# Kernel tuning notes

Hardware: AMD Instinct MI355X
Metric: run time of the kernel (lower is better)

Reference implementation:

```python
import jax, jax.numpy as jnp
import numpy as np

T, H, I, E, K = 4096, 1024, 2048, 32, 4


def setup_inputs() -> dict:
    key = jax.random.key(0)
    ks = jax.random.split(key, 8)
    s = lambda k, shape, std: (jax.random.normal(k, shape, jnp.float32) * std)
    return {
        "x": s(ks[0], (T, H), 1.0),
        "router_w": s(ks[1], (E, H), 0.02),
        "gate_w": s(ks[2], (E, H, I), 0.02),
        "up_w": s(ks[3], (E, H, I), 0.02),
        "down_w": s(ks[4], (E, I, H), 0.02),
        "shared_gate_w": s(ks[5], (H, I), 0.02),
        "shared_up_w": s(ks[6], (H, I), 0.02),
        "shared_down_w": s(ks[7], (I, H), 0.02),
        "top_k": K,
    }


def _moe_forward(x, router_w, gate_w, up_w, down_w, sg, su, sd, top_k):
    # x: [T, H]; expert weights: gate/up [E, H, I], down [E, I, H]
    Tn = x.shape[0]
    En = router_w.shape[0]

    # Router: softmax over experts, top-k selection, renormalize selected probs
    logits = x @ router_w.T                                   # [T, E]
    probs = jax.nn.softmax(logits, axis=-1)
    topk_p, topk_i = jax.lax.top_k(probs, top_k)              # [T, K]
    topk_p = topk_p / jnp.sum(topk_p, axis=-1, keepdims=True)

    # Dense combine weights: combine[t, e] = routing weight of expert e for token t
    combine = jnp.zeros((Tn, En), x.dtype).at[
        jnp.arange(Tn)[:, None], topk_i].add(topk_p)          # [T, E]

    def expert_step(acc, inp):
        wg, wu, wd, c = inp                                   # [H,I], [H,I], [I,H], [T]
        h = jax.nn.silu(x @ wg) * (x @ wu)                    # [T, I] SwiGLU
        return acc + c[:, None] * (h @ wd), None

    acc0 = jnp.zeros_like(x)
    out, _ = jax.lax.scan(expert_step, acc0,
                          (gate_w, up_w, down_w, combine.T))

    # Shared expert: always applied
    shared = (jax.nn.silu(x @ sg) * (x @ su)) @ sd            # [T, H]
    return out + shared


def reference(x, router_w, gate_w, up_w, down_w,
              shared_gate_w, shared_up_w, shared_down_w, top_k):
    return _moe_forward(x, router_w, gate_w, up_w, down_w,
                        shared_gate_w, shared_up_w, shared_down_w, top_k)
```

## Files before the change

### kernel.cpp

```cpp
#include <hip/hip_runtime.h>
#include <hip/hip_bf16.h>

#define T_TOK 4096
#define H_DIM 1024
#define I_DIM 2048
#define N_EXP 32
#define TOPK  4
#define TKTOT (T_TOK * TOPK)
#define ROWS_MAX 24576
#define MAX_TILES 192
#define BM 128
#define BK 64
#define WMAT ((size_t)I_DIM * H_DIM)

typedef _Float16 f16;
typedef __attribute__((ext_vector_type(4))) f16  f16x4;
typedef __attribute__((ext_vector_type(8))) f16  f16x8;
typedef __attribute__((ext_vector_type(4))) float f32x4;

__device__ __forceinline__ void glds16(const f16* g, f16* l) {
  __builtin_amdgcn_global_load_lds(
      (const __attribute__((address_space(1))) void*)g,
      (__attribute__((address_space(3))) void*)l, 16, 0, 0);
}
__device__ __forceinline__ void sfence() { __builtin_amdgcn_sched_barrier(0); }
__device__ __forceinline__ void bar_vm0() {
  sfence();
  asm volatile("s_waitcnt vmcnt(0) lgkmcnt(0)" ::: "memory");
  sfence();
  __builtin_amdgcn_s_barrier();
  sfence();
}

__global__ void prep_kernel(const float* __restrict__ x, f16* __restrict__ xb,
                            int* __restrict__ row_token,
                            int* __restrict__ counts) {
  int gid = blockIdx.x * blockDim.x + threadIdx.x;
  float4 v = *(const float4*)(x + (size_t)gid * 4);
  f16x4 hv = { (f16)v.x, (f16)v.y, (f16)v.z, (f16)v.w };
  *(f16x4*)(xb + (size_t)gid * 4) = hv;
  if (gid < ROWS_MAX) row_token[gid] = (gid < T_TOK) ? gid : 0;
  if (gid < N_EXP) counts[gid] = 0;
}

__global__ __launch_bounds__(256) void tcvt_kernel(
    const float* __restrict__ src, const float* __restrict__ ssrc,
    f16* __restrict__ dst, int R, int C, int tilesC) {
  int per = (R >> 6) * tilesC;
  int mat = blockIdx.x / per, rem = blockIdx.x % per;
  int r0 = (rem / tilesC) << 6, c0 = (rem % tilesC) << 6;
  const float* s = (mat < N_EXP ? src + (size_t)mat * R * C : ssrc)
                   + (size_t)r0 * C + c0;
  f16* d = dst + (size_t)mat * R * C + (size_t)c0 * R + r0;

  __shared__ float t[64][65];
  int tid = threadIdx.x;
  int rr = tid >> 2, cc = (tid & 3) * 16;
#pragma unroll
  for (int j = 0; j < 4; ++j) {
    float4 v = *(const float4*)(s + (size_t)rr * C + cc + 4 * j);
    t[rr][cc + 4 * j + 0] = v.x; t[rr][cc + 4 * j + 1] = v.y;
    t[rr][cc + 4 * j + 2] = v.z; t[rr][cc + 4 * j + 3] = v.w;
  }
  __syncthreads();
  f16x8 o0, o1;
#pragma unroll
  for (int j = 0; j < 8; ++j) o0[j] = (f16)t[cc + j][rr];
#pragma unroll
  for (int j = 0; j < 8; ++j) o1[j] = (f16)t[cc + 8 + j][rr];
  *(f16x8*)(d + (size_t)rr * R + cc) = o0;
  *(f16x8*)(d + (size_t)rr * R + cc + 8) = o1;
}

__global__ void router_kernel(const float* __restrict__ x,
                              const float* __restrict__ rw,
                              int* __restrict__ expert_sel,
                              float* __restrict__ weight_sel,
                              int* __restrict__ counts) {
  int wid = threadIdx.x >> 6, lane = threadIdx.x & 63;
  int t = blockIdx.x * 4 + wid;
  float xr[16];
#pragma unroll
  for (int j = 0; j < 16; ++j) xr[j] = x[(size_t)t * H_DIM + lane + j * 64];
  float l[32];
#pragma unroll
  for (int e = 0; e < 32; ++e) {
    float p = 0.f;
#pragma unroll
    for (int j = 0; j < 16; ++j) p += xr[j] * rw[(size_t)e * H_DIM + lane + j * 64];
#pragma unroll
    for (int off = 32; off; off >>= 1) p += __shfl_xor(p, off, 64);
    l[e] = p;
  }
  if (lane == 0) {
    unsigned used = 0;
    int sel[4]; float lv[4];
#pragma unroll
    for (int k = 0; k < 4; ++k) {
      float bv = -3.4e38f; int bi = 0;
#pragma unroll
      for (int e = 0; e < 32; ++e) {
        bool better = (((used >> e) & 1u) == 0u) && (l[e] > bv);
        bv = better ? l[e] : bv;
        bi = better ? e : bi;
      }
      used |= 1u << bi; sel[k] = bi; lv[k] = bv;
    }
    float m = lv[0];
    float p0 = __expf(lv[0] - m), p1 = __expf(lv[1] - m);
    float p2 = __expf(lv[2] - m), p3 = __expf(lv[3] - m);
    float s = p0 + p1 + p2 + p3;
    float wv[4] = { p0 / s, p1 / s, p2 / s, p3 / s };
#pragma unroll
    for (int k = 0; k < 4; ++k) {
      expert_sel[t * 4 + k] = sel[k];
      weight_sel[t * 4 + k] = wv[k];
      atomicAdd(&counts[sel[k]], 1);
    }
  }
}

__global__ void scan_kernel(const int* __restrict__ counts, int* __restrict__ cursor,
                            int* __restrict__ tile_expert, int* __restrict__ tile_row0,
                            int* __restrict__ ntiles) {
  int lane = threadIdx.x;
  if (lane < T_TOK / BM) { tile_expert[lane] = N_EXP; tile_row0[lane] = lane * BM; }
  int nte = 0, rows = 0;
  if (lane < N_EXP) {
    int c = counts[lane];
    nte = (c + BM - 1) / BM;
    rows = nte * BM;
  }
  int pnte = nte, prows = rows;
#pragma unroll
  for (int off = 1; off < 64; off <<= 1) {
    int t1 = __shfl_up(pnte, off, 64);
    int t2 = __shfl_up(prows, off, 64);
    if (lane >= off) { pnte += t1; prows += t2; }
  }
  int excl_nte = pnte - nte, excl_rows = prows - rows;
  if (lane < N_EXP) {
    int pos = T_TOK + excl_rows;
    cursor[lane] = pos;
    int tb = T_TOK / BM + excl_nte;
    for (int i = 0; i < nte; ++i) {
      tile_expert[tb + i] = lane;
      tile_row0[tb + i] = pos + i * BM;
    }
    if (lane == N_EXP - 1) ntiles[0] = tb + nte;
  }
}

__global__ void scatter_kernel(const int* __restrict__ expert_sel,
                               int* __restrict__ cursor,
                               int* __restrict__ row_token,
                               int* __restrict__ slot_of) {
  int i = blockIdx.x * blockDim.x + threadIdx.x;
  if (i >= TKTOT) return;
  int e = expert_sel[i];
  int pos = atomicAdd(&cursor[e], 1);
  row_token[pos] = i >> 2;
  slot_of[i] = pos;
}

__global__ __launch_bounds__(256, 2) void gemm1_kernel(
    const f16* __restrict__ xb,
    const f16* __restrict__ gT, const f16* __restrict__ uT,
    const int* __restrict__ row_token,
    const int* __restrict__ tile_expert, const int* __restrict__ tile_row0,
    const int* __restrict__ ntiles, f16* __restrict__ hbuf) {
  int d = blockIdx.y * gridDim.x + blockIdx.x;
  int l = (d & 7) * 768 + (d >> 3);
  int bx = l % MAX_TILES;
  int n0 = (l / MAX_TILES) * 64;
  if (bx >= ntiles[0]) return;
  int e = tile_expert[bx];
  int row0 = tile_row0[bx];
  const f16* wg = gT + (size_t)e * WMAT;
  const f16* wu = uT + (size_t)e * WMAT;

  __shared__ __align__(16) f16 smem[2 * 16384];
  f16 (*Ct)[72] = (f16(*)[72])smem;

  int tid = threadIdx.x;
  int lane = tid & 63, wid = tid >> 6;
  int wm = wid >> 1, wn = wid & 1;
  int lr = lane & 15, lk = (lane >> 4) * 8;

  const f16* abase[4];
#pragma unroll
  for (int it = 0; it < 4; ++it) {
    int idx = tid + it * 256;
    int arow = idx >> 3, sl = idx & 7;
    abase[it] = xb + (size_t)row_token[row0 + arow] * H_DIM + ((sl ^ (arow & 7)) << 3);
  }
  const f16* gbase[2];
  const f16* ubase[2];
#pragma unroll
  for (int it = 0; it < 2; ++it) {
    int idx = tid + it * 256;
    int brow = idx >> 3, sl = idx & 7;
    size_t off = (size_t)(n0 + brow) * H_DIM + ((sl ^ (brow & 7)) << 3);
    gbase[it] = wg + off;
    ubase[it] = wu + off;
  }

  f32x4 accg[4][2], accu[4][2];
#pragma unroll
  for (int m = 0; m < 4; ++m)
#pragma unroll
    for (int n = 0; n < 2; ++n) { accg[m][n] = (f32x4)0.f; accu[m][n] = (f32x4)0.f; }

  const int NK = H_DIM / BK;

#define G1_ISSUE(K0, BUF)                                                    \
  {                                                                          \
    f16* Ab = smem + (BUF) * 16384;                                          \
    f16* Bgb = Ab + 8192;                                                    \
    f16* Bub = Bgb + 4096;                                                   \
    sfence();                                                                \
    _Pragma("unroll")                                                        \
    for (int it = 0; it < 4; ++it)                                           \
      glds16(abase[it] + (K0), Ab + (tid + it * 256) * 8);                   \
    _Pragma("unroll")                                                        \
    for (int it = 0; it < 2; ++it) {                                         \
      glds16(gbase[it] + (K0), Bgb + (tid + it * 256) * 8);                  \
      glds16(ubase[it] + (K0), Bub + (tid + it * 256) * 8);                  \
    }                                                                        \
    sfence();                                                                \
  }

  G1_ISSUE(0, 0);
  for (int ks = 0; ks < NK; ++ks) {
    int buf = ks & 1;
    bar_vm0();
    if (ks + 1 < NK) G1_ISSUE((ks + 1) * BK, buf ^ 1);
    const f16* Ab = smem + buf * 16384;
    const f16* Bgb = Ab + 8192;
    const f16* Bub = Bgb + 4096;
    __builtin_amdgcn_s_setprio(1);
#pragma unroll
    for (int kk = 0; kk < BK; kk += 32) {
      f16x8 a[4], bg[2], bu[2];
#pragma unroll
      for (int m = 0; m < 4; ++m) {
        int ar = wm * 64 + m * 16 + lr;
        a[m] = *(const f16x8*)(Ab + ar * BK + ((kk + lk) ^ ((ar & 7) << 3)));
      }
#pragma unroll
      for (int n = 0; n < 2; ++n) {
        int rowb = wn * 32 + n * 16 + lr;
        int ko = (kk + lk) ^ ((rowb & 7) << 3);
        bg[n] = *(const f16x8*)(Bgb + rowb * BK + ko);
        bu[n] = *(const f16x8*)(Bub + rowb * BK + ko);
      }
#pragma unroll
      for (int m = 0; m < 4; ++m)
#pragma unroll
        for (int n = 0; n < 2; ++n) {
          accg[m][n] = __builtin_amdgcn_mfma_f32_16x16x32_f16(a[m], bg[n], accg[m][n], 0, 0, 0);
          accu[m][n] = __builtin_amdgcn_mfma_f32_16x16x32_f16(a[m], bu[n], accu[m][n], 0, 0, 0);
        }
    }
    __builtin_amdgcn_s_setprio(0);
  }
#undef G1_ISSUE

  __syncthreads();
#pragma unroll
  for (int m = 0; m < 4; ++m)
#pragma unroll
    for (int n = 0; n < 2; ++n)
#pragma unroll
      for (int j = 0; j < 4; ++j) {
        float g = accg[m][n][j], u = accu[m][n][j];
        float hv = g / (1.f + __expf(-g)) * u;
        Ct[wm * 64 + m * 16 + (lane >> 4) * 4 + j][wn * 32 + n * 16 + lr] = (f16)hv;
      }
  __syncthreads();
#pragma unroll
  for (int it = 0; it < 4; ++it) {
    int idx = tid + it * 256;
    int r = idx >> 3, g8 = (idx & 7) * 8;
    *(f16x8*)(hbuf + (size_t)(row0 + r) * I_DIM + n0 + g8) = *(const f16x8*)&Ct[r][g8];
  }
}

__global__ __launch_bounds__(256, 2) void gemm2_kernel(
    const f16* __restrict__ hbuf,
    const f16* __restrict__ dT,
    const int* __restrict__ tile_expert, const int* __restrict__ tile_row0,
    const int* __restrict__ ntiles, f16* __restrict__ ybuf) {
  int d = blockIdx.y * gridDim.x + blockIdx.x;
  int l = (d & 7) * 192 + (d >> 3);
  int bx = l % MAX_TILES;
  int n0 = (l / MAX_TILES) * 128;
  if (bx >= ntiles[0]) return;
  int e = tile_expert[bx];
  int row0 = tile_row0[bx];
  const f16* wd = dT + (size_t)e * WMAT;

  __shared__ __align__(16) f16 smem[2 * 16384];
  f16 (*Ct)[136] = (f16(*)[136])smem;

  int tid = threadIdx.x;
  int lane = tid & 63, wid = tid >> 6;
  int wm = wid >> 1, wn = wid & 1;
  int lr = lane & 15, lk = (lane >> 4) * 8;

  const f16* abase[4];
  const f16* bbase[4];
#pragma unroll
  for (int it = 0; it < 4; ++it) {
    int idx = tid + it * 256;
    int arow = idx >> 3, sl = idx & 7;
    abase[it] = hbuf + (size_t)(row0 + arow) * I_DIM + ((sl ^ (arow & 7)) << 3);
    bbase[it] = wd + (size_t)(n0 + arow) * I_DIM + ((sl ^ (arow & 7)) << 3);
  }

  f32x4 acc[4][4];
#pragma unroll
  for (int m = 0; m < 4; ++m)
#pragma unroll
    for (int n = 0; n < 4; ++n) acc[m][n] = (f32x4)0.f;

  const int NK = I_DIM / BK;

#define G2_ISSUE(K0, BUF)                                                    \
  {                                                                          \
    f16* Ab = smem + (BUF) * 16384;                                          \
    f16* Bb = Ab + 8192;                                                     \
    sfence();                                                                \
    _Pragma("unroll")                                                        \
    for (int it = 0; it < 4; ++it) {                                         \
      glds16(abase[it] + (K0), Ab + (tid + it * 256) * 8);                   \
      glds16(bbase[it] + (K0), Bb + (tid + it * 256) * 8);                   \
    }                                                                        \
    sfence();                                                                \
  }

  G2_ISSUE(0, 0);
  for (int ks = 0; ks < NK; ++ks) {
    int buf = ks & 1;
    bar_vm0();
    if (ks + 1 < NK) G2_ISSUE((ks + 1) * BK, buf ^ 1);
    const f16* Ab = smem + buf * 16384;
    const f16* Bb = Ab + 8192;
    __builtin_amdgcn_s_setprio(1);
#pragma unroll
    for (int kk = 0; kk < BK; kk += 32) {
      f16x8 a[4], bd[4];
#pragma unroll
      for (int m = 0; m < 4; ++m) {
        int ar = wm * 64 + m * 16 + lr;
        a[m] = *(const f16x8*)(Ab + ar * BK + ((kk + lk) ^ ((ar & 7) << 3)));
      }
#pragma unroll
      for (int n = 0; n < 4; ++n) {
        int rowb = wn * 64 + n * 16 + lr;
        bd[n] = *(const f16x8*)(Bb + rowb * BK + ((kk + lk) ^ ((rowb & 7) << 3)));
      }
#pragma unroll
      for (int m = 0; m < 4; ++m)
#pragma unroll
        for (int n = 0; n < 4; ++n)
          acc[m][n] = __builtin_amdgcn_mfma_f32_16x16x32_f16(a[m], bd[n], acc[m][n], 0, 0, 0);
    }
    __builtin_amdgcn_s_setprio(0);
  }
#undef G2_ISSUE

  __syncthreads();
#pragma unroll
  for (int m = 0; m < 4; ++m)
#pragma unroll
    for (int n = 0; n < 4; ++n)
#pragma unroll
      for (int j = 0; j < 4; ++j)
        Ct[wm * 64 + m * 16 + (lane >> 4) * 4 + j][wn * 64 + n * 16 + lr] =
            (f16)acc[m][n][j];
  __syncthreads();
#pragma unroll
  for (int it = 0; it < 8; ++it) {
    int idx = tid + it * 256;
    int r = idx >> 4, g8 = (idx & 15) * 8;
    *(f16x8*)(ybuf + (size_t)(row0 + r) * H_DIM + n0 + g8) = *(const f16x8*)&Ct[r][g8];
  }
}

__global__ void gather_kernel(const f16* __restrict__ ybuf,
                              const int* __restrict__ slot_of,
                              const float* __restrict__ weight_sel,
                              float* __restrict__ out) {
  int gid = blockIdx.x * blockDim.x + threadIdx.x;
  int t = gid >> 7, s8 = (gid & 127) * 8;
  f16x8 ysh = *(const f16x8*)(ybuf + (size_t)t * H_DIM + s8);
  float a[8];
#pragma unroll
  for (int j = 0; j < 8; ++j) a[j] = (float)ysh[j];
#pragma unroll
  for (int k = 0; k < 4; ++k) {
    int sl = slot_of[t * 4 + k];
    float w = weight_sel[t * 4 + k];
    f16x8 v = *(const f16x8*)(ybuf + (size_t)sl * H_DIM + s8);
#pragma unroll
    for (int j = 0; j < 8; ++j) a[j] += w * (float)v[j];
  }
  float4 o0 = { a[0], a[1], a[2], a[3] };
  float4 o1 = { a[4], a[5], a[6], a[7] };
  *(float4*)(out + (size_t)t * H_DIM + s8) = o0;
  *(float4*)(out + (size_t)t * H_DIM + s8 + 4) = o1;
}

extern "C" void kernel_launch(void* const* d_in, const int* in_sizes, int n_in,
                              void* d_out, int out_size, void* d_ws, size_t ws_size,
                              hipStream_t stream) {
  const float* x        = (const float*)d_in[0];
  const float* router_w = (const float*)d_in[1];
  const float* gate_w   = (const float*)d_in[2];
  const float* up_w     = (const float*)d_in[3];
  const float* down_w   = (const float*)d_in[4];
  const float* sgw      = (const float*)d_in[5];
  const float* suw      = (const float*)d_in[6];
  const float* sdw      = (const float*)d_in[7];
  float* out = (float*)d_out;

  char* w = (char*)d_ws;
  f16*   xb         = (f16*)w;   w += (size_t)T_TOK * H_DIM * 2;
  int*   expert_sel = (int*)w;   w += (size_t)TKTOT * 4;
  float* weight_sel = (float*)w; w += (size_t)TKTOT * 4;
  int*   slot_of    = (int*)w;   w += (size_t)TKTOT * 4;
  int*   counts     = (int*)w;   w += 256;
  int*   cursor     = (int*)w;   w += 256;
  int*   tile_exp   = (int*)w;   w += MAX_TILES * 4;
  int*   tile_row0  = (int*)w;   w += MAX_TILES * 4;
  int*   ntiles     = (int*)w;   w += 256;
  int*   row_token  = (int*)w;   w += (size_t)ROWS_MAX * 4;
  f16*   hbuf       = (f16*)w;   w += (size_t)ROWS_MAX * I_DIM * 2;
  f16*   ybuf       = (f16*)w;   w += (size_t)ROWS_MAX * H_DIM * 2;
  f16*   gT         = (f16*)w;   w += (size_t)(N_EXP + 1) * WMAT * 2;
  f16*   uT         = (f16*)w;   w += (size_t)(N_EXP + 1) * WMAT * 2;
  f16*   dT         = (f16*)w;   w += (size_t)(N_EXP + 1) * WMAT * 2;
  if ((size_t)(w - (char*)d_ws) > ws_size) return;

  prep_kernel<<<(T_TOK * H_DIM / 4) / 256, 256, 0, stream>>>(x, xb, row_token, counts);
  tcvt_kernel<<<(N_EXP + 1) * (H_DIM / 64) * (I_DIM / 64), 256, 0, stream>>>(
      gate_w, sgw, gT, H_DIM, I_DIM, I_DIM / 64);
  tcvt_kernel<<<(N_EXP + 1) * (H_DIM / 64) * (I_DIM / 64), 256, 0, stream>>>(
      up_w, suw, uT, H_DIM, I_DIM, I_DIM / 64);
  tcvt_kernel<<<(N_EXP + 1) * (I_DIM / 64) * (H_DIM / 64), 256, 0, stream>>>(
      down_w, sdw, dT, I_DIM, H_DIM, H_DIM / 64);
  router_kernel<<<T_TOK / 4, 256, 0, stream>>>(x, router_w, expert_sel, weight_sel, counts);
  scan_kernel<<<1, 64, 0, stream>>>(counts, cursor, tile_exp, tile_row0, ntiles);
  scatter_kernel<<<TKTOT / 256, 256, 0, stream>>>(expert_sel, cursor, row_token, slot_of);
  gemm1_kernel<<<dim3(MAX_TILES, I_DIM / 64), 256, 0, stream>>>(
      xb, gT, uT, row_token, tile_exp, tile_row0, ntiles, hbuf);
  gemm2_kernel<<<dim3(MAX_TILES, H_DIM / 128), 256, 0, stream>>>(
      hbuf, dT, tile_exp, tile_row0, ntiles, ybuf);
  gather_kernel<<<(T_TOK * (H_DIM / 8)) / 256, 256, 0, stream>>>(
      ybuf, slot_of, weight_sel, out);
}
```

Measured before the change: 743.1 us.

## Triple-buffer GEMM K-loop with BK=32 and partial vmcnt waits; remap gemm2 tiles

Both expert GEMM kernels move from a double-buffered BK=64 loop that drains all global-to-LDS loads each step to a triple-buffered BK=32 loop. Each step waits with vmcnt(4), so one future stage stays in flight while the current one is computed. Shared memory drops from 64 KB to 48 KB and launch bounds rise to 3 blocks per CU, aiming to hide memory latency through occupancy. gemm2 also remaps block indices so the eight N-tiles of one row tile are scheduled next to each other, for better L2 reuse of the hidden activations. The cost is twice as many barriers per K and a smaller swizzle pattern that may cause more LDS bank conflicts.

```diff
diff --git a/kernel.cpp b/kernel.cpp
--- a/kernel.cpp
+++ b/kernel.cpp
@@ -10,7 +10,7 @@
 #define ROWS_MAX 24576
 #define MAX_TILES 192
 #define BM 128
-#define BK 64
+#define BK 32
 #define WMAT ((size_t)I_DIM * H_DIM)
 
 typedef _Float16 f16;
@@ -24,6 +24,13 @@
       (__attribute__((address_space(3))) void*)l, 16, 0, 0);
 }
 __device__ __forceinline__ void sfence() { __builtin_amdgcn_sched_barrier(0); }
+__device__ __forceinline__ void bar_vm4() {
+  sfence();
+  asm volatile("s_waitcnt vmcnt(4) lgkmcnt(0)" ::: "memory");
+  sfence();
+  __builtin_amdgcn_s_barrier();
+  sfence();
+}
 __device__ __forceinline__ void bar_vm0() {
   sfence();
   asm volatile("s_waitcnt vmcnt(0) lgkmcnt(0)" ::: "memory");
@@ -163,7 +170,7 @@
   slot_of[i] = pos;
 }
 
-__global__ __launch_bounds__(256, 2) void gemm1_kernel(
+__global__ __launch_bounds__(256, 3) void gemm1_kernel(
     const f16* __restrict__ xb,
     const f16* __restrict__ gT, const f16* __restrict__ uT,
     const int* __restrict__ row_token,
@@ -179,7 +186,7 @@
   const f16* wg = gT + (size_t)e * WMAT;
   const f16* wu = uT + (size_t)e * WMAT;
 
-  __shared__ __align__(16) f16 smem[2 * 16384];
+  __shared__ __align__(16) f16 smem[3 * 8192];
   f16 (*Ct)[72] = (f16(*)[72])smem;
 
   int tid = threadIdx.x;
@@ -187,22 +194,20 @@
   int wm = wid >> 1, wn = wid & 1;
   int lr = lane & 15, lk = (lane >> 4) * 8;
 
-  const f16* abase[4];
-#pragma unroll
-  for (int it = 0; it < 4; ++it) {
-    int idx = tid + it * 256;
-    int arow = idx >> 3, sl = idx & 7;
-    abase[it] = xb + (size_t)row_token[row0 + arow] * H_DIM + ((sl ^ (arow & 7)) << 3);
-  }
-  const f16* gbase[2];
-  const f16* ubase[2];
+  const f16* abase[2];
 #pragma unroll
   for (int it = 0; it < 2; ++it) {
     int idx = tid + it * 256;
-    int brow = idx >> 3, sl = idx & 7;
-    size_t off = (size_t)(n0 + brow) * H_DIM + ((sl ^ (brow & 7)) << 3);
-    gbase[it] = wg + off;
-    ubase[it] = wu + off;
+    int arow = idx >> 2, sl = idx & 3;
+    abase[it] = xb + (size_t)row_token[row0 + arow] * H_DIM + ((sl ^ (arow & 3)) << 3);
+  }
+  const f16* gbase;
+  const f16* ubase;
+  {
+    int brow = tid >> 2, sl = tid & 3;
+    size_t off = (size_t)(n0 + brow) * H_DIM + ((sl ^ (brow & 3)) << 3);
+    gbase = wg + off;
+    ubase = wu + off;
   }
 
   f32x4 accg[4][2], accu[4][2];
@@ -215,56 +220,57 @@
 
 #define G1_ISSUE(K0, BUF)                                                    \
   {                                                                          \
-    f16* Ab = smem + (BUF) * 16384;                                          \
-    f16* Bgb = Ab + 8192;                                                    \
-    f16* Bub = Bgb + 4096;                                                   \
+    f16* Ab_ = (BUF);                                                        \
     sfence();                                                                \
-    _Pragma("unroll")                                                        \
-    for (int it = 0; it < 4; ++it)                                           \
-      glds16(abase[it] + (K0), Ab + (tid + it * 256) * 8);                   \
-    _Pragma("unroll")                                                        \
-    for (int it = 0; it < 2; ++it) {                                         \
-      glds16(gbase[it] + (K0), Bgb + (tid + it * 256) * 8);                  \
-      glds16(ubase[it] + (K0), Bub + (tid + it * 256) * 8);                  \
+    glds16(abase[0] + (K0), Ab_ + tid * 8);                                  \
+    glds16(abase[1] + (K0), Ab_ + (tid + 256) * 8);                          \
+    glds16(gbase + (K0), Ab_ + 4096 + tid * 8);                              \
+    glds16(ubase + (K0), Ab_ + 6144 + tid * 8);                              \
+    sfence();                                                                \
+  }
+
+#define G1_MFMA(BUF)                                                         \
+  {                                                                          \
+    const f16* Ab_ = (BUF);                                                  \
+    __builtin_amdgcn_s_setprio(1);                                           \
+    f16x8 a[4], bg[2], bu[2];                                                \
+    _Pragma("unroll")                                                        \
+    for (int m = 0; m < 4; ++m) {                                            \
+      int ar = wm * 64 + m * 16 + lr;                                        \
+      a[m] = *(const f16x8*)(Ab_ + ar * 32 + (lk ^ ((ar & 3) << 3)));        \
     }                                                                        \
-    sfence();                                                                \
-  }
-
-  G1_ISSUE(0, 0);
-  for (int ks = 0; ks < NK; ++ks) {
-    int buf = ks & 1;
-    bar_vm0();
-    if (ks + 1 < NK) G1_ISSUE((ks + 1) * BK, buf ^ 1);
-    const f16* Ab = smem + buf * 16384;
-    const f16* Bgb = Ab + 8192;
-    const f16* Bub = Bgb + 4096;
-    __builtin_amdgcn_s_setprio(1);
-#pragma unroll
-    for (int kk = 0; kk < BK; kk += 32) {
-      f16x8 a[4], bg[2], bu[2];
-#pragma unroll
-      for (int m = 0; m < 4; ++m) {
-        int ar = wm * 64 + m * 16 + lr;
-        a[m] = *(const f16x8*)(Ab + ar * BK + ((kk + lk) ^ ((ar & 7) << 3)));
-      }
-#pragma unroll
-      for (int n = 0; n < 2; ++n) {
-        int rowb = wn * 32 + n * 16 + lr;
-        int ko = (kk + lk) ^ ((rowb & 7) << 3);
-        bg[n] = *(const f16x8*)(Bgb + rowb * BK + ko);
-        bu[n] = *(const f16x8*)(Bub + rowb * BK + ko);
-      }
-#pragma unroll
-      for (int m = 0; m < 4; ++m)
-#pragma unroll
-        for (int n = 0; n < 2; ++n) {
-          accg[m][n] = __builtin_amdgcn_mfma_f32_16x16x32_f16(a[m], bg[n], accg[m][n], 0, 0, 0);
-          accu[m][n] = __builtin_amdgcn_mfma_f32_16x16x32_f16(a[m], bu[n], accu[m][n], 0, 0, 0);
-        }
-    }
-    __builtin_amdgcn_s_setprio(0);
-  }
-#undef G1_ISSUE
+    _Pragma("unroll")                                                        \
+    for (int n = 0; n < 2; ++n) {                                            \
+      int rowb = wn * 32 + n * 16 + lr;                                      \
+      int ko = lk ^ ((rowb & 3) << 3);                                       \
+      bg[n] = *(const f16x8*)(Ab_ + 4096 + rowb * 32 + ko);                  \
+      bu[n] = *(const f16x8*)(Ab_ + 6144 + rowb * 32 + ko);                  \
+    }                                                                        \
+    _Pragma("unroll")                                                        \
+    for (int m = 0; m < 4; ++m)                                              \
+      _Pragma("unroll")                                                      \
+      for (int n = 0; n < 2; ++n) {                                          \
+        accg[m][n] = __builtin_amdgcn_mfma_f32_16x16x32_f16(a[m], bg[n], accg[m][n], 0, 0, 0); \
+        accu[m][n] = __builtin_amdgcn_mfma_f32_16x16x32_f16(a[m], bu[n], accu[m][n], 0, 0, 0); \
+      }                                                                      \
+    __builtin_amdgcn_s_setprio(0);                                           \
+  }
+
+  f16* cur = smem;
+  f16* nxt = smem + 8192;
+  f16* nx2 = smem + 16384;
+  G1_ISSUE(0, cur);
+  G1_ISSUE(BK, nxt);
+  for (int ks = 0; ks < NK - 2; ++ks) {
+    bar_vm4();
+    G1_ISSUE((ks + 2) * BK, nx2);
+    G1_MFMA(cur);
+    f16* t = cur; cur = nxt; nxt = nx2; nx2 = t;
+  }
+  bar_vm4();
+  G1_MFMA(cur);
+  bar_vm0();
+  G1_MFMA(nxt);
 
   __syncthreads();
 #pragma unroll
@@ -284,23 +290,25 @@
     int r = idx >> 3, g8 = (idx & 7) * 8;
     *(f16x8*)(hbuf + (size_t)(row0 + r) * I_DIM + n0 + g8) = *(const f16x8*)&Ct[r][g8];
   }
-}
-
-__global__ __launch_bounds__(256, 2) void gemm2_kernel(
+#undef G1_ISSUE
+#undef G1_MFMA
+}
+
+__global__ __launch_bounds__(256, 3) void gemm2_kernel(
     const f16* __restrict__ hbuf,
     const f16* __restrict__ dT,
     const int* __restrict__ tile_expert, const int* __restrict__ tile_row0,
     const int* __restrict__ ntiles, f16* __restrict__ ybuf) {
   int d = blockIdx.y * gridDim.x + blockIdx.x;
   int l = (d & 7) * 192 + (d >> 3);
-  int bx = l % MAX_TILES;
-  int n0 = (l / MAX_TILES) * 128;
+  int bx = l >> 3;
+  int n0 = (l & 7) * 128;
   if (bx >= ntiles[0]) return;
   int e = tile_expert[bx];
   int row0 = tile_row0[bx];
   const f16* wd = dT + (size_t)e * WMAT;
 
-  __shared__ __align__(16) f16 smem[2 * 16384];
+  __shared__ __align__(16) f16 smem[3 * 8192];
   f16 (*Ct)[136] = (f16(*)[136])smem;
 
   int tid = threadIdx.x;
@@ -308,14 +316,14 @@
   int wm = wid >> 1, wn = wid & 1;
   int lr = lane & 15, lk = (lane >> 4) * 8;
 
-  const f16* abase[4];
-  const f16* bbase[4];
-#pragma unroll
-  for (int it = 0; it < 4; ++it) {
+  const f16* abase[2];
+  const f16* bbase[2];
+#pragma unroll
+  for (int it = 0; it < 2; ++it) {
     int idx = tid + it * 256;
-    int arow = idx >> 3, sl = idx & 7;
-    abase[it] = hbuf + (size_t)(row0 + arow) * I_DIM + ((sl ^ (arow & 7)) << 3);
-    bbase[it] = wd + (size_t)(n0 + arow) * I_DIM + ((sl ^ (arow & 7)) << 3);
+    int arow = idx >> 2, sl = idx & 3;
+    abase[it] = hbuf + (size_t)(row0 + arow) * I_DIM + ((sl ^ (arow & 3)) << 3);
+    bbase[it] = wd + (size_t)(n0 + arow) * I_DIM + ((sl ^ (arow & 3)) << 3);
   }
 
   f32x4 acc[4][4];
@@ -328,47 +336,53 @@
 
 #define G2_ISSUE(K0, BUF)                                                    \
   {                                                                          \
-    f16* Ab = smem + (BUF) * 16384;                                          \
-    f16* Bb = Ab + 8192;                                                     \
+    f16* Ab_ = (BUF);                                                        \
     sfence();                                                                \
-    _Pragma("unroll")                                                        \
-    for (int it = 0; it < 4; ++it) {                                         \
-      glds16(abase[it] + (K0), Ab + (tid + it * 256) * 8);                   \
-      glds16(bbase[it] + (K0), Bb + (tid + it * 256) * 8);                   \
+    glds16(abase[0] + (K0), Ab_ + tid * 8);                                  \
+    glds16(abase[1] + (K0), Ab_ + (tid + 256) * 8);                          \
+    glds16(bbase[0] + (K0), Ab_ + 4096 + tid * 8);                           \
+    glds16(bbase[1] + (K0), Ab_ + 4096 + (tid + 256) * 8);                   \
+    sfence();                                                                \
+  }
+
+#define G2_MFMA(BUF)                                                         \
+  {                                                                          \
+    const f16* Ab_ = (BUF);                                                  \
+    __builtin_amdgcn_s_setprio(1);                                           \
+    f16x8 a[4], bd[4];                                                       \
+    _Pragma("unroll")                                                        \
+    for (int m = 0; m < 4; ++m) {                                            \
+      int ar = wm * 64 + m * 16 + lr;                                        \
+      a[m] = *(const f16x8*)(Ab_ + ar * 32 + (lk ^ ((ar & 3) << 3)));        \
     }                                                                        \
-    sfence();                                                                \
-  }
-
-  G2_ISSUE(0, 0);
-  for (int ks = 0; ks < NK; ++ks) {
-    int buf = ks & 1;
-    bar_vm0();
-    if (ks + 1 < NK) G2_ISSUE((ks + 1) * BK, buf ^ 1);
-    const f16* Ab = smem + buf * 16384;
-    const f16* Bb = Ab + 8192;
-    __builtin_amdgcn_s_setprio(1);
-#pragma unroll
-    for (int kk = 0; kk < BK; kk += 32) {
-      f16x8 a[4], bd[4];
-#pragma unroll
-      for (int m = 0; m < 4; ++m) {
-        int ar = wm * 64 + m * 16 + lr;
-        a[m] = *(const f16x8*)(Ab + ar * BK + ((kk + lk) ^ ((ar & 7) << 3)));
-      }
-#pragma unroll
-      for (int n = 0; n < 4; ++n) {
-        int rowb = wn * 64 + n * 16 + lr;
-        bd[n] = *(const f16x8*)(Bb + rowb * BK + ((kk + lk) ^ ((rowb & 7) << 3)));
-      }
-#pragma unroll
-      for (int m = 0; m < 4; ++m)
-#pragma unroll
-        for (int n = 0; n < 4; ++n)
-          acc[m][n] = __builtin_amdgcn_mfma_f32_16x16x32_f16(a[m], bd[n], acc[m][n], 0, 0, 0);
-    }
-    __builtin_amdgcn_s_setprio(0);
-  }
-#undef G2_ISSUE
+    _Pragma("unroll")                                                        \
+    for (int n = 0; n < 4; ++n) {                                            \
+      int rowb = wn * 64 + n * 16 + lr;                                      \
+      bd[n] = *(const f16x8*)(Ab_ + 4096 + rowb * 32 + (lk ^ ((rowb & 3) << 3))); \
+    }                                                                        \
+    _Pragma("unroll")                                                        \
+    for (int m = 0; m < 4; ++m)                                              \
+      _Pragma("unroll")                                                      \
+      for (int n = 0; n < 4; ++n)                                            \
+        acc[m][n] = __builtin_amdgcn_mfma_f32_16x16x32_f16(a[m], bd[n], acc[m][n], 0, 0, 0); \
+    __builtin_amdgcn_s_setprio(0);                                           \
+  }
+
+  f16* cur = smem;
+  f16* nxt = smem + 8192;
+  f16* nx2 = smem + 16384;
+  G2_ISSUE(0, cur);
+  G2_ISSUE(BK, nxt);
+  for (int ks = 0; ks < NK - 2; ++ks) {
+    bar_vm4();
+    G2_ISSUE((ks + 2) * BK, nx2);
+    G2_MFMA(cur);
+    f16* t = cur; cur = nxt; nxt = nx2; nx2 = t;
+  }
+  bar_vm4();
+  G2_MFMA(cur);
+  bar_vm0();
+  G2_MFMA(nxt);
 
   __syncthreads();
 #pragma unroll
@@ -386,6 +400,8 @@
     int r = idx >> 4, g8 = (idx & 15) * 8;
     *(f16x8*)(ybuf + (size_t)(row0 + r) * H_DIM + n0 + g8) = *(const f16x8*)&Ct[r][g8];
   }
+#undef G2_ISSUE
+#undef G2_MFMA
 }
 
 __global__ void gather_kernel(const f16* __restrict__ ybuf,
```

Measured after the change: 773.4 us. 4.1% more time.
